# Optimization experiments

Hardware: AMD Instinct MI355X
Metric: run time of the kernel (lower is better)

## Reference

```python
import jax, jax.numpy as jnp
import numpy as np

L, B, E = 128, 16, 512
C_OUT = 64
KERNELS = [1, 3, 5, 7]
M = len(KERNELS) * C_OUT          # mlpdec_in = 256
OUT_SIZE = 256
SLOPE = 0.1


def setup_inputs() -> dict:
    key = jax.random.key(0)
    ks = jax.random.split(key, 32)
    s = 0.02
    d = {"x": jax.random.normal(ks[0], (L, B, E), dtype=jnp.float32)}
    # conv branches: weight (C_out, 1, k, E), bias (C_out,)
    for i, k in enumerate(KERNELS):
        d[f"cw{i}"] = jax.random.normal(ks[1 + 2 * i], (C_OUT, 1, k, E), dtype=jnp.float32) * s
        d[f"cb{i}"] = jnp.zeros((C_OUT,), dtype=jnp.float32)
    dims = [(C_OUT, 2 * M), (C_OUT, C_OUT), (C_OUT, C_OUT), (C_OUT, C_OUT)]
    for i, (o, inn) in enumerate(dims):
        d[f"mw{i}"] = jax.random.normal(ks[10 + 2 * i], (o, inn), dtype=jnp.float32) * s
        d[f"mb{i}"] = jnp.zeros((o,), dtype=jnp.float32)
    # mlp_layer: Linear(C->C), Linear(C->output_size)
    d["lw0"] = jax.random.normal(ks[20], (C_OUT, C_OUT), dtype=jnp.float32) * s
    d["lb0"] = jnp.zeros((C_OUT,), dtype=jnp.float32)
    d["lw1"] = jax.random.normal(ks[21], (OUT_SIZE, C_OUT), dtype=jnp.float32) * s
    d["lb1"] = jnp.zeros((OUT_SIZE,), dtype=jnp.float32)
    return d


def _lrelu(x):
    return jax.nn.leaky_relu(x, SLOPE)


def _conv_branch(xb, w, b):
    # xb: (B,1,L,E), w: (C,1,k,E) -> (B,C,L)
    k = w.shape[2]
    pad = (k - 1) // 2
    y = jax.lax.conv_general_dilated(
        xb, w, window_strides=(1, 1), padding=[(pad, pad), (0, 0)],
        dimension_numbers=("NCHW", "OIHW", "NCHW"))
    return _lrelu(y[..., 0] + b[None, :, None])


def reference(x, cw0, cb0, cw1, cb1, cw2, cb2, cw3, cb3,
              mw0, mb0, mw1, mb1, mw2, mb2, mw3, mb3,
              lw0, lb0, lw1, lb1):
    # x: (L,B,E) -> (B,1,L,E)
    xb = jnp.transpose(x, (1, 0, 2))[:, None, :, :]
    feats = jnp.concatenate([
        _conv_branch(xb, cw0, cb0), _conv_branch(xb, cw1, cb1),
        _conv_branch(xb, cw2, cb2), _conv_branch(xb, cw3, cb3)], axis=1)  # (B, 4C, L)
    f = jnp.transpose(feats, (2, 0, 1))  # (L, B, M)
    # pairwise: pair[i, j] = [f[j], f[i]]  -> (L, L, B, 2M)
    a = jnp.broadcast_to(f[None, :, :, :], (L, L, B, M))
    bpart = jnp.broadcast_to(f[:, None, :, :], (L, L, B, M))
    h = jnp.concatenate([a, bpart], axis=-1)
    for w, bb in ((mw0, mb0), (mw1, mb1), (mw2, mb2), (mw3, mb3)):
        h = _lrelu(h @ w.T + bb)
    h = h.sum(axis=0)  # (L, B, C)
    h = _lrelu(h @ lw0.T + lb0)
    return _lrelu(h @ lw1.T + lb1)  # (L, B, OUT_SIZE)
```

## Files before the change

### kernel.cpp

```cpp
#include <hip/hip_runtime.h>
#include <hip/hip_bf16.h>

#define SLOPE 0.1f
typedef unsigned short u16;
typedef unsigned int u32;
typedef __attribute__((ext_vector_type(8))) short short8;
typedef __attribute__((ext_vector_type(4))) float floatx4;

__device__ __forceinline__ float lrelu(float x) { return x > 0.0f ? x : SLOPE * x; }

__device__ __forceinline__ void split_rn(float x, u16* h, u16* l) {
    union { __hip_bfloat16 b; u16 u; } c1, c2;
    c1.b = __float2bfloat16(x);
    float hf = __bfloat162float(c1.b);
    c2.b = __float2bfloat16(x - hf);
    *h = c1.u; *l = c2.u;
}

__device__ __forceinline__ void pack2x2(float v0, float v1, u32& h, u32& l) {
    u32 a0 = __float_as_uint(v0), a1 = __float_as_uint(v1);
    h = __builtin_amdgcn_perm(a1, a0, 0x07060302u);
    float r0 = v0 - __uint_as_float(a0 & 0xFFFF0000u);
    float r1 = v1 - __uint_as_float(a1 & 0xFFFF0000u);
    l = __builtin_amdgcn_perm(__float_as_uint(r1), __float_as_uint(r0), 0x07060302u);
}

__device__ __forceinline__ short8 load_frag(const u16* p) {
    union { uint4 q; short8 s; } cv;
    cv.q = *(const uint4*)p;
    return cv.s;
}

__device__ __forceinline__ floatx4 mfma16(short8 a, short8 b, floatx4 c) {
    return __builtin_amdgcn_mfma_f32_16x16x32_bf16(a, b, c, 0, 0, 0);
}

__global__ __launch_bounds__(256) void p0_prep(
    const float* __restrict__ x,
    const float* __restrict__ cw0, const float* __restrict__ cw1,
    const float* __restrict__ cw2, const float* __restrict__ cw3,
    const float* __restrict__ mw0, const float* __restrict__ mw1,
    const float* __restrict__ mw2, const float* __restrict__ mw3,
    const float* __restrict__ lw0, const float* __restrict__ lw1,
    u16* __restrict__ xfh, u16* __restrict__ xfl,
    u16* __restrict__ wcfh, u16* __restrict__ wcfl,
    u16* __restrict__ b2fh, u16* __restrict__ b2fl,
    u16* __restrict__ w3fh, u16* __restrict__ w3fl,
    float* __restrict__ lw0t, float* __restrict__ lw1t)
{
    int idx = (blockIdx.x * 256 + threadIdx.x) * 4;
    if (idx < 1048576) {
        const int j = idx & 7, lane = (idx >> 3) & 63;
        const int kc = (idx >> 9) & 15, rt = idx >> 13;
        const int l15 = lane & 15, quad = lane >> 4;
        const float4 s = *(const float4*)(x + (rt * 16 + l15) * 512 + kc * 32 + quad * 8 + j);
        u16 h[4], l[4];
        split_rn(s.x, &h[0], &l[0]); split_rn(s.y, &h[1], &l[1]);
        split_rn(s.z, &h[2], &l[2]); split_rn(s.w, &h[3], &l[3]);
        *(ushort4*)(xfh + idx) = make_ushort4(h[0], h[1], h[2], h[3]);
        *(ushort4*)(xfl + idx) = make_ushort4(l[0], l[1], l[2], l[3]);
        return;
    }
    idx -= 1048576;
    if (idx < 524288) {
        const int j = idx & 7, lane = (idx >> 3) & 63;
        const int kc = (idx >> 9) & 15, nt = (idx >> 13) & 3, slot = idx >> 15;
        int branch, base;
        if (slot == 0)      { branch = 0; base = 0; }
        else if (slot < 4)  { branch = 1; base = 1; }
        else if (slot < 9)  { branch = 2; base = 4; }
        else                { branch = 3; base = 9; }
        const int dk = slot - base, ksz = 2 * branch + 1;
        const float* cw = branch == 0 ? cw0 : branch == 1 ? cw1 : branch == 2 ? cw2 : cw3;
        const int c = nt * 16 + (lane & 15);
        const int e = kc * 32 + (lane >> 4) * 8 + j;
        const float4 s = *(const float4*)(cw + (c * ksz + dk) * 512 + e);
        u16 h[4], l[4];
        split_rn(s.x, &h[0], &l[0]); split_rn(s.y, &h[1], &l[1]);
        split_rn(s.z, &h[2], &l[2]); split_rn(s.w, &h[3], &l[3]);
        *(ushort4*)(wcfh + idx) = make_ushort4(h[0], h[1], h[2], h[3]);
        *(ushort4*)(wcfl + idx) = make_ushort4(l[0], l[1], l[2], l[3]);
        return;
    }
    idx -= 524288;
    if (idx < 32768) {
        const int j = idx & 7, lane = (idx >> 3) & 63;
        const int kc = (idx >> 9) & 7, nt = (idx >> 12) & 3, nh = idx >> 14;
        const int n = nh * 64 + nt * 16 + (lane & 15);
        const int k = kc * 32 + (lane >> 4) * 8 + j;
        const float4 s = *(const float4*)(mw0 + (n & 63) * 512 + (n >> 6) * 256 + k);
        u16 h[4], l[4];
        split_rn(s.x, &h[0], &l[0]); split_rn(s.y, &h[1], &l[1]);
        split_rn(s.z, &h[2], &l[2]); split_rn(s.w, &h[3], &l[3]);
        *(ushort4*)(b2fh + idx) = make_ushort4(h[0], h[1], h[2], h[3]);
        *(ushort4*)(b2fl + idx) = make_ushort4(l[0], l[1], l[2], l[3]);
        return;
    }
    idx -= 32768;
    if (idx < 12288) {
        const int j = idx & 7, lane = (idx >> 3) & 63;
        const int kc = (idx >> 9) & 1, mt = (idx >> 10) & 3, layer = idx >> 12;
        const float* mw = layer == 0 ? mw1 : layer == 1 ? mw2 : mw3;
        const int ch = mt * 16 + (lane & 15);
        const int k = kc * 32 + (lane >> 4) * 8 + j;
        const float4 s = *(const float4*)(mw + ch * 64 + k);
        u16 h[4], l[4];
        split_rn(s.x, &h[0], &l[0]); split_rn(s.y, &h[1], &l[1]);
        split_rn(s.z, &h[2], &l[2]); split_rn(s.w, &h[3], &l[3]);
        *(ushort4*)(w3fh + idx) = make_ushort4(h[0], h[1], h[2], h[3]);
        *(ushort4*)(w3fl + idx) = make_ushort4(l[0], l[1], l[2], l[3]);
        return;
    }
    idx -= 12288;
    if (idx < 4096) {
        const int k = idx >> 6, n = idx & 63;
        float4 o;
        o.x = lw0[(n + 0) * 64 + k]; o.y = lw0[(n + 1) * 64 + k];
        o.z = lw0[(n + 2) * 64 + k]; o.w = lw0[(n + 3) * 64 + k];
        *(float4*)(lw0t + idx) = o;
        return;
    }
    idx -= 4096;
    if (idx < 16384) {
        const int k = idx >> 8, n = idx & 255;
        float4 o;
        o.x = lw1[(n + 0) * 64 + k]; o.y = lw1[(n + 1) * 64 + k];
        o.z = lw1[(n + 2) * 64 + k]; o.w = lw1[(n + 3) * 64 + k];
        *(float4*)(lw1t + idx) = o;
        return;
    }
}

__global__ __launch_bounds__(512) void k1f_conv(
    const u16* __restrict__ xfh, const u16* __restrict__ xfl,
    const u16* __restrict__ wcfh, const u16* __restrict__ wcfl,
    const float* __restrict__ cb0, const float* __restrict__ cb1,
    const float* __restrict__ cb2, const float* __restrict__ cb3,
    u16* __restrict__ Ffh, u16* __restrict__ Ffl)
{
    __shared__ float P[8][16][72];

    const int t = threadIdx.x, lane = t & 63, w = t >> 6;
    const int rtp = blockIdx.x;
    const int br = blockIdx.y;
    const int base = br * br;
    const int ksz = 2 * br + 1;
    const int l15 = lane & 15, quad = lane >> 4;

    floatx4 acc[2][4];
    #pragma unroll
    for (int r = 0; r < 2; ++r)
        #pragma unroll
        for (int j = 0; j < 4; ++j) acc[r][j] = (floatx4)0.0f;

    const int nunits = ksz * 16;
    for (int unit = w; unit < nunits; unit += 8) {
        const int dk = unit >> 4, kc = unit & 15;
        const int slot = base + dk;
        short8 bh[4], bl[4];
        #pragma unroll
        for (int nt = 0; nt < 4; ++nt) {
            const int boff = (((slot * 4 + nt) * 16 + kc) * 64 + lane) * 8;
            bh[nt] = load_frag(wcfh + boff);
            bl[nt] = load_frag(wcfl + boff);
        }
        #pragma unroll
        for (int r = 0; r < 2; ++r) {
            const int rts = rtp + r * 64 + dk - br;
            if (rts < 0 || rts >= 128) continue;
            const int aoff = ((rts * 16 + kc) * 64 + lane) * 8;
            const short8 ah = load_frag(xfh + aoff);
            const short8 al = load_frag(xfl + aoff);
            #pragma unroll
            for (int nt = 0; nt < 4; ++nt) {
                acc[r][nt] = mfma16(ah, bh[nt], acc[r][nt]);
                acc[r][nt] = mfma16(ah, bl[nt], acc[r][nt]);
                acc[r][nt] = mfma16(al, bh[nt], acc[r][nt]);
            }
        }
    }

    const float* cb = br == 0 ? cb0 : br == 1 ? cb1 : br == 2 ? cb2 : cb3;
    #pragma unroll
    for (int r = 0; r < 2; ++r) {
        #pragma unroll
        for (int nt = 0; nt < 4; ++nt)
            #pragma unroll
            for (int rr = 0; rr < 4; ++rr)
                P[w][quad * 4 + rr][nt * 16 + l15] = acc[r][nt][rr];
        __syncthreads();
        if (t < 256) {
            const int row = t >> 4, c4 = (t & 15) * 4;
            u16 h4[4], l4[4];
            #pragma unroll
            for (int i = 0; i < 4; ++i) {
                float val = cb[c4 + i];
                #pragma unroll
                for (int ww = 0; ww < 8; ++ww) val += P[ww][row][c4 + i];
                split_rn(lrelu(val), &h4[i], &l4[i]);
            }
            const int rt = rtp + r * 64;
            const int m4 = br * 64 + c4;
            const int dst = ((rt * 8 + (m4 >> 5)) * 64 + ((m4 >> 3) & 3) * 16 + row) * 8 + (m4 & 7);
            *(ushort4*)(Ffh + dst) = make_ushort4(h4[0], h4[1], h4[2], h4[3]);
            *(ushort4*)(Ffl + dst) = make_ushort4(l4[0], l4[1], l4[2], l4[3]);
        }
        __syncthreads();
    }
}

__global__ __launch_bounds__(256) void k2_uv(
    const u16* __restrict__ Ffh, const u16* __restrict__ Ffl,
    const u16* __restrict__ b2fh, const u16* __restrict__ b2fl,
    const float* __restrict__ mb0,
    float* __restrict__ u, float* __restrict__ v_t)
{
    __shared__ float P[4][16][72];

    const int t = threadIdx.x, lane = t & 63, w = t >> 6;
    const int rt = blockIdx.x;
    const int nh = blockIdx.y;
    const int l15 = lane & 15, quad = lane >> 4;

    floatx4 acc[4];
    #pragma unroll
    for (int j = 0; j < 4; ++j) acc[j] = (floatx4)0.0f;

    #pragma unroll
    for (int kk = 0; kk < 2; ++kk) {
        const int kc = w * 2 + kk;
        const int aoff = ((rt * 8 + kc) * 64 + lane) * 8;
        const short8 ah = load_frag(Ffh + aoff);
        const short8 al = load_frag(Ffl + aoff);
        #pragma unroll
        for (int nt = 0; nt < 4; ++nt) {
            const int boff = (((nh * 4 + nt) * 8 + kc) * 64 + lane) * 8;
            const short8 bh = load_frag(b2fh + boff);
            const short8 bl = load_frag(b2fl + boff);
            acc[nt] = mfma16(ah, bh, acc[nt]);
            acc[nt] = mfma16(ah, bl, acc[nt]);
            acc[nt] = mfma16(al, bh, acc[nt]);
        }
    }

    #pragma unroll
    for (int nt = 0; nt < 4; ++nt)
        #pragma unroll
        for (int r = 0; r < 4; ++r)
            P[w][quad * 4 + r][nt * 16 + l15] = acc[nt][r];
    __syncthreads();

    const int row = t >> 4, c4 = (t & 15) * 4;
    const int rglob = rt * 16 + row;
    float4 oo;
    #pragma unroll
    for (int i = 0; i < 4; ++i)
        (&oo.x)[i] = P[0][row][c4 + i] + P[1][row][c4 + i]
                   + P[2][row][c4 + i] + P[3][row][c4 + i];
    if (nh == 0) {
        oo.x += mb0[c4 + 0]; oo.y += mb0[c4 + 1];
        oo.z += mb0[c4 + 2]; oo.w += mb0[c4 + 3];
        *(float4*)(u + rglob * 64 + c4) = oo;
    } else {
        const int i = rglob >> 4, b = rglob & 15;
        *(float4*)(v_t + (b * 128 + i) * 64 + c4) = oo;
    }
}

__global__ __launch_bounds__(256, 4) void k3_pair(
    const float* __restrict__ u, const float* __restrict__ v_t,
    const u16* __restrict__ w3fh, const u16* __restrict__ w3fl,
    const float* __restrict__ mb1, const float* __restrict__ mb2,
    const float* __restrict__ mb3,
    const float* __restrict__ lw0t, const float* __restrict__ lb0,
    const float* __restrict__ lw1t, const float* __restrict__ lb1,
    float* __restrict__ out)
{
    __shared__ __align__(16) u16 Hh[128][72];
    __shared__ __align__(16) u16 Hl[128][72];
    __shared__ float Sp[4][64];
    __shared__ float Ss[64];
    __shared__ float T1[64];

    const int t = threadIdx.x, lane = t & 63, w = t >> 6;
    const int jb = blockIdx.x, b = jb & 15;
    const int l15 = lane & 15, quad = lane >> 4;
    const int i0 = w * 32;
    const int c4 = l15 * 4;

    const float4 uu = *(const float4*)(u + jb * 64 + c4);

    const float* vb = v_t + (b * 128 + i0) * 64;
    #pragma unroll
    for (int n = 0; n < 8; ++n) {
        const int idx = n * 64 + lane;
        const int il = idx >> 4;
        const float4 vv = *(const float4*)(vb + idx * 4);
        const float a0 = lrelu(vv.x + uu.x), a1 = lrelu(vv.y + uu.y);
        const float a2 = lrelu(vv.z + uu.z), a3 = lrelu(vv.w + uu.w);
        u32 h01, l01, h23, l23;
        pack2x2(a0, a1, h01, l01);
        pack2x2(a2, a3, h23, l23);
        *(uint2*)&Hh[i0 + il][c4] = make_uint2(h01, h23);
        *(uint2*)&Hl[i0 + il][c4] = make_uint2(l01, l23);
    }

    const float* mbp[3] = {mb1, mb2, mb3};
    for (int layer = 0; layer < 3; ++layer) {
        floatx4 acc[4][2];
        #pragma unroll
        for (int i = 0; i < 4; ++i)
            #pragma unroll
            for (int j = 0; j < 2; ++j) acc[i][j] = (floatx4)0.0f;

        #pragma unroll
        for (int kc = 0; kc < 2; ++kc) {
            short8 ah[4], al[4];
            #pragma unroll
            for (int mt = 0; mt < 4; ++mt) {
                const int aoff = (((layer * 4 + mt) * 2 + kc) * 64 + lane) * 8;
                ah[mt] = load_frag(w3fh + aoff);
                al[mt] = load_frag(w3fl + aoff);
            }
            const int k0 = kc * 32 + quad * 8;
            #pragma unroll
            for (int nt = 0; nt < 2; ++nt) {
                const short8 bh = load_frag(&Hh[i0 + nt * 16 + l15][k0]);
                const short8 bl = load_frag(&Hl[i0 + nt * 16 + l15][k0]);
                #pragma unroll
                for (int mt = 0; mt < 4; ++mt) {
                    acc[mt][nt] = mfma16(ah[mt], bh, acc[mt][nt]);
                    acc[mt][nt] = mfma16(ah[mt], bl, acc[mt][nt]);
                    acc[mt][nt] = mfma16(al[mt], bh, acc[mt][nt]);
                }
            }
        }

        if (layer < 2) {
            #pragma unroll
            for (int mt = 0; mt < 4; ++mt) {
                float bias[4];
                #pragma unroll
                for (int r = 0; r < 4; ++r) bias[r] = mbp[layer][mt * 16 + quad * 4 + r];
                #pragma unroll
                for (int nt = 0; nt < 2; ++nt) {
                    const int i = i0 + nt * 16 + l15;
                    const float v0 = lrelu(acc[mt][nt][0] + bias[0]);
                    const float v1 = lrelu(acc[mt][nt][1] + bias[1]);
                    const float v2 = lrelu(acc[mt][nt][2] + bias[2]);
                    const float v3 = lrelu(acc[mt][nt][3] + bias[3]);
                    u32 h01, l01, h23, l23;
                    pack2x2(v0, v1, h01, l01);
                    pack2x2(v2, v3, h23, l23);
                    *(uint2*)&Hh[i][mt * 16 + quad * 4] = make_uint2(h01, h23);
                    *(uint2*)&Hl[i][mt * 16 + quad * 4] = make_uint2(l01, l23);
                }
            }
        } else {
            #pragma unroll
            for (int mt = 0; mt < 4; ++mt) {
                float bias[4];
                #pragma unroll
                for (int r = 0; r < 4; ++r) bias[r] = mbp[2][mt * 16 + quad * 4 + r];
                float4 sv;
                #pragma unroll
                for (int r = 0; r < 4; ++r) {
                    float val = lrelu(acc[mt][0][r] + bias[r])
                              + lrelu(acc[mt][1][r] + bias[r]);
                    val += __shfl_xor(val, 1, 16);
                    val += __shfl_xor(val, 2, 16);
                    val += __shfl_xor(val, 4, 16);
                    val += __shfl_xor(val, 8, 16);
                    (&sv.x)[r] = val;
                }
                if (l15 == 0)
                    *(float4*)(&Sp[w][mt * 16 + quad * 4]) = sv;
            }
        }
    }

    __syncthreads();
    if (t < 64) Ss[t] = Sp[0][t] + Sp[1][t] + Sp[2][t] + Sp[3][t];
    __syncthreads();
    if (t < 64) {
        float a = lb0[t];
        #pragma unroll 8
        for (int k = 0; k < 64; ++k) a += Ss[k] * lw0t[k * 64 + t];
        T1[t] = lrelu(a);
    }
    __syncthreads();
    {
        float a = lb1[t];
        #pragma unroll 8
        for (int k = 0; k < 64; ++k) a += T1[k] * lw1t[k * 256 + t];
        out[jb * 256 + t] = lrelu(a);
    }
}

extern "C" void kernel_launch(void* const* d_in, const int* in_sizes, int n_in,
                              void* d_out, int out_size, void* d_ws, size_t ws_size,
                              hipStream_t stream)
{
    const float* x   = (const float*)d_in[0];
    const float* cw0 = (const float*)d_in[1];
    const float* cb0 = (const float*)d_in[2];
    const float* cw1 = (const float*)d_in[3];
    const float* cb1 = (const float*)d_in[4];
    const float* cw2 = (const float*)d_in[5];
    const float* cb2 = (const float*)d_in[6];
    const float* cw3 = (const float*)d_in[7];
    const float* cb3 = (const float*)d_in[8];
    const float* mw0 = (const float*)d_in[9];
    const float* mb0 = (const float*)d_in[10];
    const float* mw1 = (const float*)d_in[11];
    const float* mb1 = (const float*)d_in[12];
    const float* mw2 = (const float*)d_in[13];
    const float* mb2 = (const float*)d_in[14];
    const float* mw3 = (const float*)d_in[15];
    const float* mb3 = (const float*)d_in[16];
    const float* lw0 = (const float*)d_in[17];
    const float* lb0 = (const float*)d_in[18];
    const float* lw1 = (const float*)d_in[19];
    const float* lb1 = (const float*)d_in[20];
    float* out = (float*)d_out;

    char* base = (char*)d_ws;
    u16* xfh   = (u16*)(base + 0);
    u16* xfl   = (u16*)(base + 2097152);
    u16* wcfh  = (u16*)(base + 4194304);
    u16* wcfl  = (u16*)(base + 5242880);
    u16* b2fh  = (u16*)(base + 6291456);
    u16* b2fl  = (u16*)(base + 6356992);
    u16* w3fh  = (u16*)(base + 6422528);
    u16* w3fl  = (u16*)(base + 6447104);
    float* lw0t  = (float*)(base + 6471680);
    float* lw1t  = (float*)(base + 6488064);
    u16* Ffh   = (u16*)(base + 6553600);
    u16* Ffl   = (u16*)(base + 7602176);
    float* u   = (float*)(base + 8650752);
    float* v_t = (float*)(base + 9175040);

    hipLaunchKernelGGL(p0_prep, dim3(1600), dim3(256), 0, stream,
                       x, cw0, cw1, cw2, cw3, mw0, mw1, mw2, mw3, lw0, lw1,
                       xfh, xfl, wcfh, wcfl, b2fh, b2fl, w3fh, w3fl, lw0t, lw1t);
    hipLaunchKernelGGL(k1f_conv, dim3(64, 4), dim3(512), 0, stream,
                       xfh, xfl, wcfh, wcfl, cb0, cb1, cb2, cb3, Ffh, Ffl);
    hipLaunchKernelGGL(k2_uv, dim3(128, 2), dim3(256), 0, stream,
                       Ffh, Ffl, b2fh, b2fl, mb0, u, v_t);
    hipLaunchKernelGGL(k3_pair, dim3(2048), dim3(256), 0, stream,
                       u, v_t, w3fh, w3fl, mb1, mb2, mb3, lw0t, lb0, lw1t, lb1, out);
}
```

Baseline: 156.0 us.

## Split conv across kernel-offset slots and reduce partials in the uv kernel

The conv kernel's grid grows from one block per branch to one block per (branch, tap offset) slot, 16 in all, so the k=7 branch no longer serialises seven taps inside one block and the work is spread evenly. Each block writes fp32 partial sums to a new workspace buffer. The uv kernel then adds the partials over the taps, applies bias and leaky ReLU, and does the bf16 hi/lo split before its MFMAs. This buys more conv parallelism and better load balance at the cost of extra global traffic for the partials (about 8 MB) and redundant reduction work in k2.

After: 151.9 us. -2.6%, faster.

```diff
diff --git a/kernel.cpp b/kernel.cpp
--- a/kernel.cpp
+++ b/kernel.cpp
@@ -134,17 +134,19 @@
 __global__ __launch_bounds__(512) void k1f_conv(
     const u16* __restrict__ xfh, const u16* __restrict__ xfl,
     const u16* __restrict__ wcfh, const u16* __restrict__ wcfl,
-    const float* __restrict__ cb0, const float* __restrict__ cb1,
-    const float* __restrict__ cb2, const float* __restrict__ cb3,
-    u16* __restrict__ Ffh, u16* __restrict__ Ffl)
+    float* __restrict__ Fp)
 {
     __shared__ float P[8][16][72];
 
     const int t = threadIdx.x, lane = t & 63, w = t >> 6;
     const int rtp = blockIdx.x;
-    const int br = blockIdx.y;
-    const int base = br * br;
-    const int ksz = 2 * br + 1;
+    const int slot = blockIdx.y;
+    int br, base;
+    if (slot == 0)      { br = 0; base = 0; }
+    else if (slot < 4)  { br = 1; base = 1; }
+    else if (slot < 9)  { br = 2; base = 4; }
+    else                { br = 3; base = 9; }
+    const int dk = slot - base;
     const int l15 = lane & 15, quad = lane >> 4;
 
     floatx4 acc[2][4];
@@ -153,10 +155,9 @@
         #pragma unroll
         for (int j = 0; j < 4; ++j) acc[r][j] = (floatx4)0.0f;
 
-    const int nunits = ksz * 16;
-    for (int unit = w; unit < nunits; unit += 8) {
-        const int dk = unit >> 4, kc = unit & 15;
-        const int slot = base + dk;
+    #pragma unroll
+    for (int kk = 0; kk < 2; ++kk) {
+        const int kc = w * 2 + kk;
         short8 bh[4], bl[4];
         #pragma unroll
         for (int nt = 0; nt < 4; ++nt) {
@@ -180,7 +181,6 @@
         }
     }
 
-    const float* cb = br == 0 ? cb0 : br == 1 ? cb1 : br == 2 ? cb2 : cb3;
     #pragma unroll
     for (int r = 0; r < 2; ++r) {
         #pragma unroll
@@ -191,27 +191,26 @@
         __syncthreads();
         if (t < 256) {
             const int row = t >> 4, c4 = (t & 15) * 4;
-            u16 h4[4], l4[4];
+            float4 o;
             #pragma unroll
             for (int i = 0; i < 4; ++i) {
-                float val = cb[c4 + i];
-                #pragma unroll
-                for (int ww = 0; ww < 8; ++ww) val += P[ww][row][c4 + i];
-                split_rn(lrelu(val), &h4[i], &l4[i]);
-            }
-            const int rt = rtp + r * 64;
-            const int m4 = br * 64 + c4;
-            const int dst = ((rt * 8 + (m4 >> 5)) * 64 + ((m4 >> 3) & 3) * 16 + row) * 8 + (m4 & 7);
-            *(ushort4*)(Ffh + dst) = make_ushort4(h4[0], h4[1], h4[2], h4[3]);
-            *(ushort4*)(Ffl + dst) = make_ushort4(l4[0], l4[1], l4[2], l4[3]);
+                float val = P[0][row][c4 + i];
+                #pragma unroll
+                for (int ww = 1; ww < 8; ++ww) val += P[ww][row][c4 + i];
+                (&o.x)[i] = val;
+            }
+            const int rowg = (rtp + r * 64) * 16 + row;
+            *(float4*)(Fp + (slot * 2048 + rowg) * 64 + c4) = o;
         }
         __syncthreads();
     }
 }
 
 __global__ __launch_bounds__(256) void k2_uv(
-    const u16* __restrict__ Ffh, const u16* __restrict__ Ffl,
+    const float* __restrict__ Fp,
     const u16* __restrict__ b2fh, const u16* __restrict__ b2fl,
+    const float* __restrict__ cb0, const float* __restrict__ cb1,
+    const float* __restrict__ cb2, const float* __restrict__ cb3,
     const float* __restrict__ mb0,
     float* __restrict__ u, float* __restrict__ v_t)
 {
@@ -229,9 +228,30 @@
     #pragma unroll
     for (int kk = 0; kk < 2; ++kk) {
         const int kc = w * 2 + kk;
-        const int aoff = ((rt * 8 + kc) * 64 + lane) * 8;
-        const short8 ah = load_frag(Ffh + aoff);
-        const short8 al = load_frag(Ffl + aoff);
+        const int br = kc >> 1;
+        const int base = br * br, ksz = 2 * br + 1;
+        const int cc0 = (kc & 1) * 32 + quad * 8;
+        const int row = rt * 16 + l15;
+
+        float s[8];
+        #pragma unroll
+        for (int j = 0; j < 8; ++j) s[j] = 0.0f;
+        for (int d = 0; d < ksz; ++d) {
+            const float* p = Fp + ((base + d) * 2048 + row) * 64 + cc0;
+            const float4 q0 = *(const float4*)p;
+            const float4 q1 = *(const float4*)(p + 4);
+            s[0] += q0.x; s[1] += q0.y; s[2] += q0.z; s[3] += q0.w;
+            s[4] += q1.x; s[5] += q1.y; s[6] += q1.z; s[7] += q1.w;
+        }
+        const float* cb = br == 0 ? cb0 : br == 1 ? cb1 : br == 2 ? cb2 : cb3;
+        union { u16 us[8]; short8 v; } AH, AL;
+        #pragma unroll
+        for (int j = 0; j < 8; ++j) {
+            const float val = lrelu(s[j] + cb[cc0 + j]);
+            split_rn(val, &AH.us[j], &AL.us[j]);
+        }
+        const short8 ah = AH.v, al = AL.v;
+
         #pragma unroll
         for (int nt = 0; nt < 4; ++nt) {
             const int boff = (((nh * 4 + nt) * 8 + kc) * 64 + lane) * 8;
@@ -435,18 +455,17 @@
     u16* w3fl  = (u16*)(base + 6447104);
     float* lw0t  = (float*)(base + 6471680);
     float* lw1t  = (float*)(base + 6488064);
-    u16* Ffh   = (u16*)(base + 6553600);
-    u16* Ffl   = (u16*)(base + 7602176);
-    float* u   = (float*)(base + 8650752);
-    float* v_t = (float*)(base + 9175040);
+    float* Fp  = (float*)(base + 6553600);
+    float* u   = (float*)(base + 14942208);
+    float* v_t = (float*)(base + 15466496);
 
     hipLaunchKernelGGL(p0_prep, dim3(1600), dim3(256), 0, stream,
                        x, cw0, cw1, cw2, cw3, mw0, mw1, mw2, mw3, lw0, lw1,
                        xfh, xfl, wcfh, wcfl, b2fh, b2fl, w3fh, w3fl, lw0t, lw1t);
-    hipLaunchKernelGGL(k1f_conv, dim3(64, 4), dim3(512), 0, stream,
-                       xfh, xfl, wcfh, wcfl, cb0, cb1, cb2, cb3, Ffh, Ffl);
+    hipLaunchKernelGGL(k1f_conv, dim3(64, 16), dim3(512), 0, stream,
+                       xfh, xfl, wcfh, wcfl, Fp);
     hipLaunchKernelGGL(k2_uv, dim3(128, 2), dim3(256), 0, stream,
-                       Ffh, Ffl, b2fh, b2fl, mb0, u, v_t);
+                       Fp, b2fh, b2fl, cb0, cb1, cb2, cb3, mb0, u, v_t);
     hipLaunchKernelGGL(k3_pair, dim3(2048), dim3(256), 0, stream,
                        u, v_t, w3fh, w3fl, mb1, mb2, mb3, lw0t, lb0, lw1t, lb1, out);
 }
```
